# Kernel tuning notes

Measured on AMD Instinct MI355X. Metric: run time of the kernel, lower is better.

Reference implementation:

```python
import jax, jax.numpy as jnp
import numpy as np

WH, WW = 7, 7
N = WH * WW            # 49 tokens per window
DIM = 128
HEADS = 4
HEAD_DIM = DIM // HEADS
SCALE = HEAD_DIM ** -0.5
NW = 1024              # windows per image (224/7)^2
B = 16                 # images
B_ = B * NW


def _relative_position_index():
    ch, cw = np.meshgrid(np.arange(WH), np.arange(WW), indexing='ij')
    coords = np.stack([ch, cw]).reshape(2, -1)          # [2, N]
    rel = coords[:, :, None] - coords[:, None, :]        # [2, N, N]
    rel = rel.transpose(1, 2, 0)
    rel[:, :, 0] += WH - 1
    rel[:, :, 1] += WW - 1
    rel[:, :, 0] *= 2 * WW - 1
    return rel.sum(-1).astype(np.int32)                 # [N, N]


def setup_inputs() -> dict:
    key = jax.random.key(0)
    ks = jax.random.split(key, 5)
    x = jax.random.normal(ks[0], (B_, N, DIM), dtype=jnp.float32)
    mask = jnp.zeros((NW, N, N), dtype=jnp.float32)
    qkv_w = jax.random.normal(ks[1], (3 * DIM, DIM), dtype=jnp.float32) * (DIM ** -0.5)
    qkv_b = jnp.zeros((3 * DIM,), dtype=jnp.float32)
    proj_w = jax.random.normal(ks[2], (DIM, DIM), dtype=jnp.float32) * (DIM ** -0.5)
    proj_b = jnp.zeros((DIM,), dtype=jnp.float32)
    rel_bias_table = jax.random.normal(ks[3], ((2 * WH - 1) * (2 * WW - 1), HEADS), dtype=jnp.float32) * 0.02
    rel_index = jnp.asarray(_relative_position_index())
    return {"x": x, "mask": mask, "qkv_w": qkv_w, "qkv_b": qkv_b,
            "proj_w": proj_w, "proj_b": proj_b,
            "rel_bias_table": rel_bias_table, "rel_index": rel_index}


def reference(x, mask, qkv_w, qkv_b, proj_w, proj_b, rel_bias_table, rel_index):
    Bw, n, c = x.shape
    # fused qkv projection: [B_, N, 3, H, hd]
    qkv = (x @ qkv_w.T + qkv_b).reshape(Bw, n, 3, HEADS, HEAD_DIM)
    qkv = jnp.transpose(qkv, (2, 0, 3, 1, 4))            # [3, B_, H, N, hd]
    q, k, v = qkv[0], qkv[1], qkv[2]
    attn = jnp.einsum('bhnd,bhmd->bhnm', q * SCALE, k)   # [B_, H, N, N]
    # gathered relative position bias: [N, N, H] -> [H, N, N]
    bias = rel_bias_table[rel_index.reshape(-1)].reshape(n, n, HEADS)
    attn = attn + jnp.transpose(bias, (2, 0, 1))[None]
    # additive per-window mask
    nW = mask.shape[0]
    attn = attn.reshape(Bw // nW, nW, HEADS, n, n) + mask[None, :, None]
    attn = jax.nn.softmax(attn.reshape(Bw, HEADS, n, n), axis=-1)
    out = jnp.einsum('bhnm,bhmd->bhnd', attn, v)         # [B_, H, N, hd]
    out = jnp.transpose(out, (0, 2, 1, 3)).reshape(Bw, n, c)
    return out @ proj_w.T + proj_b
```

## Files before the change

kernel.cpp:

```cpp
#include <hip/hip_runtime.h>
#include <hip/hip_bf16.h>


#define NTOK 49
#define NP   64
#define DIMC 128
#define HEADS 4
#define HD   32
#define NWM  1024
#define SCALE 0.17677669529663687f

typedef __attribute__((ext_vector_type(8))) __bf16 bf16x8;
typedef __attribute__((ext_vector_type(4))) float f32x4;

#define OFF_Q  0
#define OFF_K  12544
#define OFF_P  0
#define OFF_XB 25088
#define OFF_AO 25088
#define OFF_VT 41472
#define SMEM_BYTES 57856

__device__ __forceinline__ unsigned short f2bf(float f) {
  union { float f; unsigned u; } x; x.f = f;
  unsigned r = x.u + 0x7fffu + ((x.u >> 16) & 1u);
  return (unsigned short)(r >> 16);
}

__device__ __forceinline__ f32x4 mfma16(bf16x8 a, bf16x8 b, f32x4 c) {
  return __builtin_amdgcn_mfma_f32_16x16x32_bf16(a, b, c, 0, 0, 0);
}

__global__ void winattn_prep(const float* __restrict__ qkv_w,
                             const float* __restrict__ proj_w,
                             const float* __restrict__ table,
                             const int* __restrict__ ridx,
                             unsigned short* __restrict__ qkv_wb,
                             unsigned short* __restrict__ proj_wb,
                             float* __restrict__ bias_g) {
  int i = blockIdx.x * 256 + threadIdx.x;
  if (i < 384 * DIMC) qkv_wb[i] = f2bf(qkv_w[i]);
  if (i < DIMC * DIMC) proj_wb[i] = f2bf(proj_w[i]);
  if (i < HEADS * 64 * 64) {
    int h = i >> 12, n = (i >> 6) & 63, m = i & 63;
    float v = -1e30f;
    if (n < NTOK && m < NTOK) v = table[ridx[n * NTOK + m] * HEADS + h];
    bias_g[i] = v;
  }
}

__launch_bounds__(256, 2)
__global__ void winattn_main(const float* __restrict__ x,
                             const float* __restrict__ mask,
                             const unsigned short* __restrict__ qkv_wb,
                             const float* __restrict__ qkv_b,
                             const unsigned short* __restrict__ proj_wb,
                             const float* __restrict__ proj_b,
                             const float* __restrict__ bias_g,
                             float* __restrict__ out) {
  __shared__ char smem[SMEM_BYTES] __attribute__((aligned(128)));
  const int tid  = threadIdx.x;
  const int w    = blockIdx.x;
  const int lane = tid & 63;
  const int wid  = tid >> 6;
  const int lr   = lane & 15;
  const int lg   = lane >> 4;
  const f32x4 fzero = {0.f, 0.f, 0.f, 0.f};

  const float* xw = x + (size_t)w * (NTOK * DIMC);

  for (int i = tid; i < NTOK * 32; i += 256) {
    int n = i >> 5, c4 = i & 31;
    float4 v = *reinterpret_cast<const float4*>(xw + n * DIMC + c4 * 4);
    unsigned lo = (unsigned)f2bf(v.x) | ((unsigned)f2bf(v.y) << 16);
    unsigned hi = (unsigned)f2bf(v.z) | ((unsigned)f2bf(v.w) << 16);
    int mb = (c4 * 8) ^ ((n & 7) << 4);
    *reinterpret_cast<uint2*>(smem + OFF_XB + n * 256 + mb) = make_uint2(lo, hi);
  }
  for (int i = tid; i < (NP - NTOK) * 32; i += 256) {
    int n = NTOK + (i >> 5), c4 = i & 31;
    int mb = (c4 * 8) ^ ((n & 7) << 4);
    *reinterpret_cast<uint2*>(smem + OFF_XB + n * 256 + mb) = make_uint2(0u, 0u);
  }
  __syncthreads();

  {
    bf16x8 af[4][4];
#pragma unroll
    for (int mt = 0; mt < 4; ++mt)
#pragma unroll
      for (int kk = 0; kk < 4; ++kk) {
        int n = mt * 16 + lr;
        int mb = (kk * 64 + lg * 16) ^ ((n & 7) << 4);
        af[mt][kk] = *reinterpret_cast<const bf16x8*>(smem + OFF_XB + n * 256 + mb);
      }
    const int cb = wid * 96;
#pragma unroll
    for (int nt = 0; nt < 6; ++nt) {
      const int o = cb + nt * 16 + lr;
      const unsigned short* wrow = qkv_wb + o * DIMC;
      bf16x8 bf[4];
#pragma unroll
      for (int kk = 0; kk < 4; ++kk)
        bf[kk] = *reinterpret_cast<const bf16x8*>(wrow + kk * 32 + lg * 8);
      f32x4 acc[4];
#pragma unroll
      for (int mt = 0; mt < 4; ++mt) acc[mt] = fzero;
#pragma unroll
      for (int kk = 0; kk < 4; ++kk)
#pragma unroll
        for (int mt = 0; mt < 4; ++mt)
          acc[mt] = mfma16(af[mt][kk], bf[kk], acc[mt]);
      const float bq = qkv_b[o];
      const int s = o >> 7;
      const int h = (o & 127) >> 5;
      const int d = o & 31;
#pragma unroll
      for (int mt = 0; mt < 4; ++mt)
#pragma unroll
        for (int r = 0; r < 4; ++r) {
          const int n = mt * 16 + lg * 4 + r;
          const unsigned short bv = f2bf(acc[mt][r] + bq);
          if (s == 2) {
            int mb = (n * 2) ^ ((d & 7) << 4);
            *reinterpret_cast<unsigned short*>(smem + OFF_VT + (h * 32 + d) * 128 + mb) = bv;
          } else if (n < NTOK) {
            int base = (s == 0) ? OFF_Q : OFF_K;
            int mb = (d * 2) ^ ((n & 3) << 4);
            *reinterpret_cast<unsigned short*>(smem + base + (h * NTOK + n) * 64 + mb) = bv;
          }
        }
    }
  }
  __syncthreads();

  {
    const int h = wid;
    bf16x8 qf[4], kf[4];
#pragma unroll
    for (int mt = 0; mt < 4; ++mt) {
      int n = mt * 16 + lr; if (n > 48) n = 48;
      int mb = (lg * 16) ^ ((n & 3) << 4);
      qf[mt] = *reinterpret_cast<const bf16x8*>(smem + OFF_Q + (h * NTOK + n) * 64 + mb);
    }
#pragma unroll
    for (int nt = 0; nt < 4; ++nt) {
      int m = nt * 16 + lr; if (m > 48) m = 48;
      int mb = (lg * 16) ^ ((m & 3) << 4);
      kf[nt] = *reinterpret_cast<const bf16x8*>(smem + OFF_K + (h * NTOK + m) * 64 + mb);
    }
    f32x4 sc[4][4];
#pragma unroll
    for (int mt = 0; mt < 4; ++mt)
#pragma unroll
      for (int nt = 0; nt < 4; ++nt)
        sc[mt][nt] = mfma16(qf[mt], kf[nt], fzero);

    const float* bgh = bias_g + h * 4096;
    const float* mw  = mask + (size_t)(w & (NWM - 1)) * (NTOK * NTOK);
#pragma unroll
    for (int mt = 0; mt < 4; ++mt)
#pragma unroll
      for (int r = 0; r < 4; ++r) {
        const int n  = mt * 16 + lg * 4 + r;
        const int nc = (n > 48) ? 48 : n;
#pragma unroll
        for (int nt = 0; nt < 4; ++nt) {
          const int m  = nt * 16 + lr;
          const int mc = (m > 48) ? 48 : m;
          sc[mt][nt][r] = sc[mt][nt][r] * SCALE + bgh[n * 64 + m] + mw[nc * NTOK + mc];
        }
      }
    __syncthreads();

#pragma unroll
    for (int mt = 0; mt < 4; ++mt)
#pragma unroll
      for (int r = 0; r < 4; ++r) {
        float mx = sc[mt][0][r];
#pragma unroll
        for (int nt = 1; nt < 4; ++nt) mx = fmaxf(mx, sc[mt][nt][r]);
        mx = fmaxf(mx, __shfl_xor(mx, 1, 16));
        mx = fmaxf(mx, __shfl_xor(mx, 2, 16));
        mx = fmaxf(mx, __shfl_xor(mx, 4, 16));
        mx = fmaxf(mx, __shfl_xor(mx, 8, 16));
        float e[4]; float sum = 0.f;
#pragma unroll
        for (int nt = 0; nt < 4; ++nt) { e[nt] = __expf(sc[mt][nt][r] - mx); sum += e[nt]; }
        sum += __shfl_xor(sum, 1, 16);
        sum += __shfl_xor(sum, 2, 16);
        sum += __shfl_xor(sum, 4, 16);
        sum += __shfl_xor(sum, 8, 16);
        const float inv = __builtin_amdgcn_rcpf(sum);
        const int n = mt * 16 + lg * 4 + r;
        if (n < NTOK) {
#pragma unroll
          for (int nt = 0; nt < 4; ++nt) {
            const int m = nt * 16 + lr;
            int mb = (m * 2) ^ ((n & 7) << 4);
            *reinterpret_cast<unsigned short*>(smem + OFF_P + (h * NTOK + n) * 128 + mb) =
                f2bf(e[nt] * inv);
          }
        }
      }
  }

  {
    const int h = wid;
    bf16x8 pa[4][2], vb[2][2];
#pragma unroll
    for (int mt = 0; mt < 4; ++mt)
#pragma unroll
      for (int kk = 0; kk < 2; ++kk) {
        int n = mt * 16 + lr; if (n > 48) n = 48;
        int mb = (kk * 64 + lg * 16) ^ ((n & 7) << 4);
        pa[mt][kk] = *reinterpret_cast<const bf16x8*>(smem + OFF_P + (h * NTOK + n) * 128 + mb);
      }
#pragma unroll
    for (int dt = 0; dt < 2; ++dt)
#pragma unroll
      for (int kk = 0; kk < 2; ++kk) {
        const int d = dt * 16 + lr;
        int mb = (kk * 64 + lg * 16) ^ ((d & 7) << 4);
        vb[dt][kk] = *reinterpret_cast<const bf16x8*>(smem + OFF_VT + (h * 32 + d) * 128 + mb);
      }
    f32x4 oc[4][2];
#pragma unroll
    for (int mt = 0; mt < 4; ++mt)
#pragma unroll
      for (int dt = 0; dt < 2; ++dt) oc[mt][dt] = fzero;
#pragma unroll
    for (int kk = 0; kk < 2; ++kk)
#pragma unroll
      for (int mt = 0; mt < 4; ++mt)
#pragma unroll
        for (int dt = 0; dt < 2; ++dt)
          oc[mt][dt] = mfma16(pa[mt][kk], vb[dt][kk], oc[mt][dt]);
#pragma unroll
    for (int mt = 0; mt < 4; ++mt)
#pragma unroll
      for (int dt = 0; dt < 2; ++dt)
#pragma unroll
        for (int r = 0; r < 4; ++r) {
          const int n = mt * 16 + lg * 4 + r;
          if (n < NTOK) {
            const int c = h * 32 + dt * 16 + lr;
            int mb = (c * 2) ^ ((n & 7) << 4);
            *reinterpret_cast<unsigned short*>(smem + OFF_AO + n * 256 + mb) = f2bf(oc[mt][dt][r]);
          }
        }
  }
  __syncthreads();

  {
    bf16x8 aof[4][4];
#pragma unroll
    for (int mt = 0; mt < 4; ++mt)
#pragma unroll
      for (int kk = 0; kk < 4; ++kk) {
        int n = mt * 16 + lr; if (n > 48) n = 48;
        int mb = (kk * 64 + lg * 16) ^ ((n & 7) << 4);
        aof[mt][kk] = *reinterpret_cast<const bf16x8*>(smem + OFF_AO + n * 256 + mb);
      }
    float* ow = out + (size_t)w * (NTOK * DIMC);
#pragma unroll
    for (int ct2 = 0; ct2 < 2; ++ct2) {
      const int c = (wid * 2 + ct2) * 16 + lr;
      const unsigned short* wrow = proj_wb + c * DIMC;
      bf16x8 wb[4];
#pragma unroll
      for (int kk = 0; kk < 4; ++kk)
        wb[kk] = *reinterpret_cast<const bf16x8*>(wrow + kk * 32 + lg * 8);
      f32x4 acc[4];
#pragma unroll
      for (int mt = 0; mt < 4; ++mt) acc[mt] = fzero;
#pragma unroll
      for (int kk = 0; kk < 4; ++kk)
#pragma unroll
        for (int mt = 0; mt < 4; ++mt)
          acc[mt] = mfma16(aof[mt][kk], wb[kk], acc[mt]);
      const float bp = proj_b[c];
#pragma unroll
      for (int mt = 0; mt < 4; ++mt)
#pragma unroll
        for (int r = 0; r < 4; ++r) {
          const int n = mt * 16 + lg * 4 + r;
          if (n < NTOK) ow[n * DIMC + c] = acc[mt][r] + bp;
        }
    }
  }
}

extern "C" void kernel_launch(void* const* d_in, const int* in_sizes, int n_in,
                              void* d_out, int out_size, void* d_ws, size_t ws_size,
                              hipStream_t stream) {
  const float* x      = (const float*)d_in[0];
  const float* mask   = (const float*)d_in[1];
  const float* qkv_w  = (const float*)d_in[2];
  const float* qkv_b  = (const float*)d_in[3];
  const float* proj_w = (const float*)d_in[4];
  const float* proj_b = (const float*)d_in[5];
  const float* table  = (const float*)d_in[6];
  const int*   ridx   = (const int*)d_in[7];

  unsigned short* qkv_wb  = (unsigned short*)d_ws;
  unsigned short* proj_wb = qkv_wb + 384 * DIMC;
  float*          bias_g  = (float*)(proj_wb + DIMC * DIMC);

  winattn_prep<<<192, 256, 0, stream>>>(qkv_w, proj_w, table, ridx,
                                        qkv_wb, proj_wb, bias_g);

  const int nwin = in_sizes[0] / (NTOK * DIMC);
  winattn_main<<<nwin, 256, 0, stream>>>(x, mask, qkv_wb, qkv_b, proj_wb,
                                         proj_b, bias_g, (float*)d_out);
}
```

Measured before the change: 642.2 us.

## Shrink shared memory by aliasing buffers to raise occupancy to four blocks

Shared memory drops from about 57.9KB to 39.4KB. The V-transpose buffer now aliases the x-bf16 and attention-output region, which needs an extra barrier after x is loaded into registers and another before the AO write. The padded x rows are no longer stored; they are zeroed in registers, and V uses an unswizzled 112-byte row pitch. Launch bounds ask for 4 blocks per CU to hide latency better, at the cost of added syncs, tighter register limits and possible LDS bank conflicts on the unswizzled V layout.

```diff
diff --git a/kernel.cpp b/kernel.cpp
--- a/kernel.cpp
+++ b/kernel.cpp
@@ -3,10 +3,8 @@
 
 
 #define NTOK 49
-#define NP   64
 #define DIMC 128
 #define HEADS 4
-#define HD   32
 #define NWM  1024
 #define SCALE 0.17677669529663687f
 
@@ -17,9 +15,9 @@
 #define OFF_K  12544
 #define OFF_P  0
 #define OFF_XB 25088
+#define OFF_VT 25088
 #define OFF_AO 25088
-#define OFF_VT 41472
-#define SMEM_BYTES 57856
+#define SMEM_BYTES 39440
 
 __device__ __forceinline__ unsigned short f2bf(float f) {
   union { float f; unsigned u; } x; x.f = f;
@@ -29,6 +27,13 @@
 
 __device__ __forceinline__ f32x4 mfma16(bf16x8 a, bf16x8 b, f32x4 c) {
   return __builtin_amdgcn_mfma_f32_16x16x32_bf16(a, b, c, 0, 0, 0);
+}
+
+__device__ __forceinline__ bf16x8 zero8() {
+  bf16x8 z;
+#pragma unroll
+  for (int j = 0; j < 8; ++j) z[j] = (__bf16)0.f;
+  return z;
 }
 
 __global__ void winattn_prep(const float* __restrict__ qkv_w,
@@ -49,7 +54,7 @@
   }
 }
 
-__launch_bounds__(256, 2)
+__launch_bounds__(256, 4)
 __global__ void winattn_main(const float* __restrict__ x,
                              const float* __restrict__ mask,
                              const unsigned short* __restrict__ qkv_wb,
@@ -69,31 +74,37 @@
 
   const float* xw = x + (size_t)w * (NTOK * DIMC);
 
-  for (int i = tid; i < NTOK * 32; i += 256) {
-    int n = i >> 5, c4 = i & 31;
-    float4 v = *reinterpret_cast<const float4*>(xw + n * DIMC + c4 * 4);
-    unsigned lo = (unsigned)f2bf(v.x) | ((unsigned)f2bf(v.y) << 16);
-    unsigned hi = (unsigned)f2bf(v.z) | ((unsigned)f2bf(v.w) << 16);
-    int mb = (c4 * 8) ^ ((n & 7) << 4);
-    *reinterpret_cast<uint2*>(smem + OFF_XB + n * 256 + mb) = make_uint2(lo, hi);
-  }
-  for (int i = tid; i < (NP - NTOK) * 32; i += 256) {
-    int n = NTOK + (i >> 5), c4 = i & 31;
-    int mb = (c4 * 8) ^ ((n & 7) << 4);
-    *reinterpret_cast<uint2*>(smem + OFF_XB + n * 256 + mb) = make_uint2(0u, 0u);
-  }
+  for (int i = tid; i < NTOK * 16; i += 256) {
+    int n = i >> 4, c8 = i & 15;
+    float4 v0 = *reinterpret_cast<const float4*>(xw + n * DIMC + c8 * 8);
+    float4 v1 = *reinterpret_cast<const float4*>(xw + n * DIMC + c8 * 8 + 4);
+    uint4 d;
+    d.x = (unsigned)f2bf(v0.x) | ((unsigned)f2bf(v0.y) << 16);
+    d.y = (unsigned)f2bf(v0.z) | ((unsigned)f2bf(v0.w) << 16);
+    d.z = (unsigned)f2bf(v1.x) | ((unsigned)f2bf(v1.y) << 16);
+    d.w = (unsigned)f2bf(v1.z) | ((unsigned)f2bf(v1.w) << 16);
+    int mb = (c8 * 16) ^ ((n & 7) << 4);
+    *reinterpret_cast<uint4*>(smem + OFF_XB + n * 256 + mb) = d;
+  }
+  if (tid == 0)
+    *reinterpret_cast<uint4*>(smem + SMEM_BYTES - 16) = make_uint4(0u, 0u, 0u, 0u);
   __syncthreads();
 
+  bf16x8 af[4][4];
+#pragma unroll
+  for (int mt = 0; mt < 4; ++mt)
+#pragma unroll
+    for (int kk = 0; kk < 4; ++kk) {
+      int n = mt * 16 + lr;
+      bool pad = (n > 48);
+      if (pad) n = 48;
+      int mb = (kk * 64 + 16 * lg) ^ ((n & 7) << 4);
+      bf16x8 v = *reinterpret_cast<const bf16x8*>(smem + OFF_XB + n * 256 + mb);
+      af[mt][kk] = pad ? zero8() : v;
+    }
+  __syncthreads();
+
   {
-    bf16x8 af[4][4];
-#pragma unroll
-    for (int mt = 0; mt < 4; ++mt)
-#pragma unroll
-      for (int kk = 0; kk < 4; ++kk) {
-        int n = mt * 16 + lr;
-        int mb = (kk * 64 + lg * 16) ^ ((n & 7) << 4);
-        af[mt][kk] = *reinterpret_cast<const bf16x8*>(smem + OFF_XB + n * 256 + mb);
-      }
     const int cb = wid * 96;
 #pragma unroll
     for (int nt = 0; nt < 6; ++nt) {
@@ -112,9 +123,9 @@
         for (int mt = 0; mt < 4; ++mt)
           acc[mt] = mfma16(af[mt][kk], bf[kk], acc[mt]);
       const float bq = qkv_b[o];
-      const int s = o >> 7;
-      const int h = (o & 127) >> 5;
-      const int d = o & 31;
+      const int s  = o >> 7;
+      const int h2 = (o & 127) >> 5;
+      const int d  = o & 31;
 #pragma unroll
       for (int mt = 0; mt < 4; ++mt)
 #pragma unroll
@@ -122,20 +133,22 @@
           const int n = mt * 16 + lg * 4 + r;
           const unsigned short bv = f2bf(acc[mt][r] + bq);
           if (s == 2) {
-            int mb = (n * 2) ^ ((d & 7) << 4);
-            *reinterpret_cast<unsigned short*>(smem + OFF_VT + (h * 32 + d) * 128 + mb) = bv;
+            if (n < 56)
+              *reinterpret_cast<unsigned short*>(
+                  smem + OFF_VT + (h2 * 32 + d) * 112 + n * 2) = bv;
           } else if (n < NTOK) {
             int base = (s == 0) ? OFF_Q : OFF_K;
             int mb = (d * 2) ^ ((n & 3) << 4);
-            *reinterpret_cast<unsigned short*>(smem + base + (h * NTOK + n) * 64 + mb) = bv;
+            *reinterpret_cast<unsigned short*>(
+                smem + base + (h2 * NTOK + n) * 64 + mb) = bv;
           }
         }
     }
   }
   __syncthreads();
 
+  const int h = wid;
   {
-    const int h = wid;
     bf16x8 qf[4], kf[4];
 #pragma unroll
     for (int mt = 0; mt < 4; ++mt) {
@@ -206,7 +219,6 @@
   }
 
   {
-    const int h = wid;
     bf16x8 pa[4][2], vb[2][2];
 #pragma unroll
     for (int mt = 0; mt < 4; ++mt)
@@ -221,8 +233,8 @@
 #pragma unroll
       for (int kk = 0; kk < 2; ++kk) {
         const int d = dt * 16 + lr;
-        int mb = (kk * 64 + lg * 16) ^ ((d & 7) << 4);
-        vb[dt][kk] = *reinterpret_cast<const bf16x8*>(smem + OFF_VT + (h * 32 + d) * 128 + mb);
+        vb[dt][kk] = *reinterpret_cast<const bf16x8*>(
+            smem + OFF_VT + (h * 32 + d) * 112 + kk * 64 + 16 * lg);
       }
     f32x4 oc[4][2];
 #pragma unroll
@@ -236,6 +248,7 @@
 #pragma unroll
         for (int dt = 0; dt < 2; ++dt)
           oc[mt][dt] = mfma16(pa[mt][kk], vb[dt][kk], oc[mt][dt]);
+    __syncthreads();
 #pragma unroll
     for (int mt = 0; mt < 4; ++mt)
 #pragma unroll
@@ -246,7 +259,8 @@
           if (n < NTOK) {
             const int c = h * 32 + dt * 16 + lr;
             int mb = (c * 2) ^ ((n & 7) << 4);
-            *reinterpret_cast<unsigned short*>(smem + OFF_AO + n * 256 + mb) = f2bf(oc[mt][dt][r]);
+            *reinterpret_cast<unsigned short*>(smem + OFF_AO + n * 256 + mb) =
+                f2bf(oc[mt][dt][r]);
           }
         }
   }
@@ -259,13 +273,14 @@
 #pragma unroll
       for (int kk = 0; kk < 4; ++kk) {
         int n = mt * 16 + lr; if (n > 48) n = 48;
-        int mb = (kk * 64 + lg * 16) ^ ((n & 7) << 4);
-        aof[mt][kk] = *reinterpret_cast<const bf16x8*>(smem + OFF_AO + n * 256 + mb);
+        int s16 = 4 * kk + lg;
+        aof[mt][kk] = *reinterpret_cast<const bf16x8*>(
+            smem + OFF_AO + n * 256 + (((s16 & 8) | ((s16 ^ (n & 7)) & 7)) << 4));
       }
     float* ow = out + (size_t)w * (NTOK * DIMC);
 #pragma unroll
-    for (int ct2 = 0; ct2 < 2; ++ct2) {
-      const int c = (wid * 2 + ct2) * 16 + lr;
+    for (int ct = 0; ct < 2; ++ct) {
+      const int c = (wid * 2 + ct) * 16 + lr;
       const unsigned short* wrow = proj_wb + c * DIMC;
       bf16x8 wb[4];
 #pragma unroll
```

Result: faster. 549.1 us (-14.5%).
